# Kernel optimization log

Hardware: AMD Instinct MI355X
Metric: run time of the kernel (lower is better)

## Reference

```python
import jax, jax.numpy as jnp
import numpy as np

N, D, NH, NC, B, NL = 400, 256, 4, 2, 64, 2
HD = D // NH


def _ln(x, g, b, eps=1e-5):
    mu = x.mean(-1, keepdims=True)
    var = ((x - mu) ** 2).mean(-1, keepdims=True)
    return (x - mu) * jax.lax.rsqrt(var + eps) * g + b


def _mha(q, kv, wqkv, bqkv, wo, bo):
    # torch nn.MultiheadAttention (batch_first), eval mode
    wq, wk, wv = jnp.split(wqkv, 3, axis=0)
    bq, bk, bv = jnp.split(bqkv, 3, axis=0)
    Bsz, Sq, _ = q.shape
    Sk = kv.shape[1]
    qh = (q @ wq.T + bq).reshape(Bsz, Sq, NH, HD).transpose(0, 2, 1, 3)
    kh = (kv @ wk.T + bk).reshape(Bsz, Sk, NH, HD).transpose(0, 2, 1, 3)
    vh = (kv @ wv.T + bv).reshape(Bsz, Sk, NH, HD).transpose(0, 2, 1, 3)
    scores = jnp.einsum('bhqd,bhkd->bhqk', qh, kh) / jnp.sqrt(jnp.float32(HD))
    attn = jax.nn.softmax(scores, axis=-1)
    o = jnp.einsum('bhqk,bhkd->bhqd', attn, vh)
    o = o.transpose(0, 2, 1, 3).reshape(Bsz, Sq, D)
    return o @ wo.T + bo


def setup_inputs() -> dict:
    key = jax.random.key(0)
    ks = iter(jax.random.split(key, 64))
    w = lambda *s: (jax.random.normal(next(ks), s, dtype=jnp.float32) * 0.02)
    inp = {
        'fc_matrix': jax.random.uniform(next(ks), (B, N, N), dtype=jnp.float32),
        'sc_matrix': jax.random.uniform(next(ks), (B, N, N), dtype=jnp.float32),
        'proj_w': w(D, N), 'proj_b': jnp.zeros((D,), jnp.float32),
        'enc_qkv_w': w(NL, 3 * D, D), 'enc_qkv_b': jnp.zeros((NL, 3 * D), jnp.float32),
        'enc_out_w': w(NL, D, D), 'enc_out_b': jnp.zeros((NL, D), jnp.float32),
        'enc_lin1_w': w(NL, 4 * D, D), 'enc_lin1_b': jnp.zeros((NL, 4 * D), jnp.float32),
        'enc_lin2_w': w(NL, D, 4 * D), 'enc_lin2_b': jnp.zeros((NL, D), jnp.float32),
        'enc_n1_g': jnp.ones((NL, D), jnp.float32), 'enc_n1_b': jnp.zeros((NL, D), jnp.float32),
        'enc_n2_g': jnp.ones((NL, D), jnp.float32), 'enc_n2_b': jnp.zeros((NL, D), jnp.float32),
        'gcn_w1': w(D, N), 'gcn_b1': jnp.zeros((D,), jnp.float32),
        'gcn_w2': w(D, D), 'gcn_b2': jnp.zeros((D,), jnp.float32),
        'ca1_qkv_w': w(3 * D, D), 'ca1_qkv_b': jnp.zeros((3 * D,), jnp.float32),
        'ca1_out_w': w(D, D), 'ca1_out_b': jnp.zeros((D,), jnp.float32),
        'ca1_n_g': jnp.ones((D,), jnp.float32), 'ca1_n_b': jnp.zeros((D,), jnp.float32),
        'ca2_qkv_w': w(3 * D, D), 'ca2_qkv_b': jnp.zeros((3 * D,), jnp.float32),
        'ca2_out_w': w(D, D), 'ca2_out_b': jnp.zeros((D,), jnp.float32),
        'ca2_n_g': jnp.ones((D,), jnp.float32), 'ca2_n_b': jnp.zeros((D,), jnp.float32),
        'cls_w1': w(128, N * D), 'cls_b1': jnp.zeros((128,), jnp.float32),
        'cls_w2': w(NC, 128), 'cls_b2': jnp.zeros((NC,), jnp.float32),
    }
    return inp


def reference(fc_matrix, sc_matrix, proj_w, proj_b,
              enc_qkv_w, enc_qkv_b, enc_out_w, enc_out_b,
              enc_lin1_w, enc_lin1_b, enc_lin2_w, enc_lin2_b,
              enc_n1_g, enc_n1_b, enc_n2_g, enc_n2_b,
              gcn_w1, gcn_b1, gcn_w2, gcn_b2,
              ca1_qkv_w, ca1_qkv_b, ca1_out_w, ca1_out_b, ca1_n_g, ca1_n_b,
              ca2_qkv_w, ca2_qkv_b, ca2_out_w, ca2_out_b, ca2_n_g, ca2_n_b,
              cls_w1, cls_b1, cls_w2, cls_b2):
    # ---- FC branch: input proj + 2 post-norm transformer encoder layers ----
    h = fc_matrix @ proj_w.T + proj_b  # [B,N,D]
    for l in range(NL):
        a = _mha(h, h, enc_qkv_w[l], enc_qkv_b[l], enc_out_w[l], enc_out_b[l])
        h = _ln(h + a, enc_n1_g[l], enc_n1_b[l])
        ff = jax.nn.relu(h @ enc_lin1_w[l].T + enc_lin1_b[l]) @ enc_lin2_w[l].T + enc_lin2_b[l]
        h = _ln(h + ff, enc_n2_g[l], enc_n2_b[l])
    Z_F = h

    # ---- SC branch: dense-equivalent of per-sample nonzero()+GCNConv ----
    # all entries of sc are nonzero -> edge set == dense adjacency (self-loops present,
    # so add_remaining_self_loops is a no-op). deg = in-degree (column sums of weights).
    deg = sc_matrix.sum(axis=-2)  # [B,N]
    dinv = jnp.where(deg > 0, jax.lax.rsqrt(deg), 0.0)
    An = dinv[:, :, None] * sc_matrix * dinv[:, None, :]  # An[b,i,j] = dinv_i * w_ij * dinv_j
    h1 = jnp.einsum('bij,bid->bjd', An, sc_matrix @ gcn_w1.T) + gcn_b1  # aggregate src->dst
    h1 = jax.nn.relu(h1)
    Z_S = jnp.einsum('bij,bid->bjd', An, h1 @ gcn_w2.T) + gcn_b2  # [B,N,D]

    # ---- Cross attention (eval: dropout = identity) ----
    Z_F_cross = _ln(Z_F + _mha(Z_F, Z_S, ca1_qkv_w, ca1_qkv_b, ca1_out_w, ca1_out_b), ca1_n_g, ca1_n_b)
    Z_S_cross = _ln(Z_S + _mha(Z_S, Z_F, ca2_qkv_w, ca2_qkv_b, ca2_out_w, ca2_out_b), ca2_n_g, ca2_n_b)

    Z_joint = (Z_F_cross + Z_S_cross) * 0.5
    flat = Z_joint.reshape(Z_joint.shape[0], -1)  # [B, N*D]
    logits = jax.nn.relu(flat @ cls_w1.T + cls_b1) @ cls_w2.T + cls_b2
    return logits
```

## Files before the change

kernel.cpp:

```cpp
#include <hip/hip_runtime.h>
#include <math.h>

#define NB   64
#define NN   400
#define DD   256
#define NHH  4
#define HDD  64
#define MR   25600

typedef __attribute__((ext_vector_type(8))) short bf16x8;
typedef __attribute__((ext_vector_type(4))) float f32x4;

__device__ __forceinline__ short f2bf(float x) {
    union { float f; unsigned u; } v; v.f = x;
    return (short)((v.u + 0x7FFFu + ((v.u >> 16) & 1u)) >> 16);
}
__device__ __forceinline__ float bf2f(short s) {
    union { unsigned u; float f; } v; v.u = ((unsigned)(unsigned short)s) << 16;
    return v.f;
}
__device__ __forceinline__ void gl_lds16(const void* g, void* l) {
    __builtin_amdgcn_global_load_lds(
        (const __attribute__((address_space(1))) unsigned*)g,
        (__attribute__((address_space(3))) unsigned*)l, 16, 0, 0);
}
__device__ __forceinline__ void wait_vmcnt(int n) {
    switch (n) {
    case 0: asm volatile("s_waitcnt vmcnt(0)" ::: "memory"); break;
    case 1: asm volatile("s_waitcnt vmcnt(1)" ::: "memory"); break;
    case 2: asm volatile("s_waitcnt vmcnt(2)" ::: "memory"); break;
    case 3: asm volatile("s_waitcnt vmcnt(3)" ::: "memory"); break;
    case 4: asm volatile("s_waitcnt vmcnt(4)" ::: "memory"); break;
    default: asm volatile("s_waitcnt vmcnt(5)" ::: "memory"); break;
    }
}
__device__ __forceinline__ void barrier_raw() {
    __builtin_amdgcn_sched_barrier(0);
    __builtin_amdgcn_s_barrier();
    __builtin_amdgcn_sched_barrier(0);
}


__global__ __launch_bounds__(512, 4) void gemm_p8(
    const short* __restrict__ A, int arows, long long sA,
    const short* __restrict__ B, int brows, long long sB,
    const float* __restrict__ bias,
    short* __restrict__ C, int crows, int crz, long long sCe,
    int M, int N, int Npad, int K, int relu)
{
    __shared__ short lds[36864];
    const int tid = threadIdx.x;

    const unsigned gx = gridDim.x, gy = gridDim.y;
    const unsigned nwg = gx * gy * gridDim.z;
    const unsigned lin = (blockIdx.z * gy + blockIdx.y) * gx + blockIdx.x;
    const unsigned g = (lin & 7) * (nwg >> 3) + (lin >> 3);
    const unsigned zz = g / (gx * gy);
    const unsigned rem2 = g - zz * gx * gy;
    const unsigned mx = rem2 / gy;
    const unsigned ny = rem2 - mx * gy;

    const int z = (int)zz;
    const int m0 = (int)mx * 256, n0 = (int)ny * 128;
    const short* Ab = A + (size_t)z * sA;
    const short* Bb = B + (size_t)z * sB;

    const int w = tid >> 6, lane = tid & 63;
    const int quad = lane >> 4, l15 = lane & 15;
    const int wm = w & 3, wn = w >> 2;

    f32x4 acc[4][4] = {};

    const int KT = K >> 5;

    auto STAGE = [&](int buf, int kt) {
        const int gp0 = kt << 2;
        short* Al = lds + buf * 12288;
        short* Bl = Al + 8192;
#pragma unroll
        for (int i = 0; i < 3; ++i) {
            int c = i * 8 + w;
            if (c < 16) {
                int p = c >> 2, hh = c & 3;
                gl_lds16(Ab + ((size_t)(gp0 + p) * arows + m0 + hh * 64 + lane) * 8,
                         &Al[(p * 256 + hh * 64) * 8]);
            } else {
                int cb = c - 16, p = cb >> 1, hh = cb & 1;
                gl_lds16(Bb + ((size_t)(gp0 + p) * brows + n0 + hh * 64 + lane) * 8,
                         &Bl[(p * 128 + hh * 64) * 8]);
            }
        }
    };

    STAGE(0, 0);
    STAGE(1, 1);
    for (int kt = 0; kt < KT; ++kt) {
        wait_vmcnt(kt + 1 < KT ? 3 : 0);
        barrier_raw();
        if (kt + 2 < KT) STAGE((kt + 2) % 3, kt + 2);
        const short* Al = lds + (kt % 3) * 12288;
        const short* Bl = Al + 8192;
        bf16x8 af[4], bfr[4];
#pragma unroll
        for (int mi = 0; mi < 4; ++mi)
            af[mi] = *reinterpret_cast<const bf16x8*>(
                &Al[(quad * 256 + wm * 64 + mi * 16 + l15) * 8]);
#pragma unroll
        for (int ni = 0; ni < 4; ++ni)
            bfr[ni] = *reinterpret_cast<const bf16x8*>(
                &Bl[(quad * 128 + wn * 64 + ni * 16 + l15) * 8]);
#pragma unroll
        for (int mi = 0; mi < 4; ++mi)
#pragma unroll
            for (int ni = 0; ni < 4; ++ni)
                acc[mi][ni] = __builtin_amdgcn_mfma_f32_16x16x32_bf16(af[mi], bfr[ni], acc[mi][ni], 0, 0, 0);
    }
    __syncthreads();

#pragma unroll
    for (int mi = 0; mi < 4; ++mi) {
#pragma unroll
        for (int r = 0; r < 4; ++r) {
            int row = wm * 64 + mi * 16 + quad * 4 + r;
#pragma unroll
            for (int ni = 0; ni < 4; ++ni) {
                int col = wn * 64 + ni * 16 + l15;
                int gcol = n0 + col;
                float v = 0.0f;
                if (gcol < N) {
                    v = acc[mi][ni][r];
                    if (bias) v += bias[gcol];
                    if (relu) v = fmaxf(v, 0.0f);
                }
                lds[row * 136 + col] = f2bf(v);
            }
        }
    }
    __syncthreads();
    short* Cbz = C + (size_t)z * sCe;
    const long long zr = (long long)z * crz;
#pragma unroll
    for (int t = 0; t < 8; ++t) {
        int c = t * 512 + tid;
        int row = c & 255, p16 = c >> 8;
        int grow = m0 + row;
        int gcol0 = n0 + p16 * 8;
        if (grow < M && gcol0 < Npad) {
            bf16x8 v = *reinterpret_cast<const bf16x8*>(&lds[row * 136 + p16 * 8]);
            *reinterpret_cast<bf16x8*>(
                &Cbz[((size_t)(gcol0 >> 3) * crows + zr + grow) * 8]) = v;
        }
    }
}

__global__ __launch_bounds__(512, 4) void gemm_ln(
    const short* __restrict__ A,
    const short* __restrict__ B, int brows,
    const float* __restrict__ bias,
    const short* __restrict__ resid,
    const float* __restrict__ g, const float* __restrict__ bb,
    short* __restrict__ out, int K)
{
    __shared__ short lds[30720];
    __shared__ float gs[256], bs[256], bi_s[256];
    __shared__ float red[2][8][64];
    const int tid = threadIdx.x;
    const int m0 = blockIdx.x * 64;
    const int w = tid >> 6, lane = tid & 63;
    const int quad = lane >> 4, l15 = lane & 15;
    if (tid < 256) { gs[tid] = g[tid]; bs[tid] = bb[tid]; bi_s[tid] = bias[tid]; }

    f32x4 acc[4][2] = {};
    const int KT = K >> 5;
    const int myloads = (w < 4) ? 3 : 2;

    auto STAGE = [&](int buf, int kt) {
        const int gp0 = kt << 2;
        short* Al = lds + buf * 10240;
        short* Bl = Al + 2048;
#pragma unroll
        for (int i = 0; i < 3; ++i) {
            int c = i * 8 + w;
            if (c < 4) {
                gl_lds16(A + ((size_t)(gp0 + c) * MR + m0 + lane) * 8, &Al[(c * 64) * 8]);
            } else if (c < 20) {
                int cb = c - 4, p = cb >> 2, cq = cb & 3;
                gl_lds16(B + ((size_t)(gp0 + p) * brows + cq * 64 + lane) * 8,
                         &Bl[(p * 256 + cq * 64) * 8]);
            }
        }
    };

    STAGE(0, 0);
    STAGE(1, 1);
    for (int kt = 0; kt < KT; ++kt) {
        wait_vmcnt(kt + 1 < KT ? myloads : 0);
        barrier_raw();
        if (kt + 2 < KT) STAGE((kt + 2) % 3, kt + 2);
        const short* Al = lds + (kt % 3) * 10240;
        const short* Bl = Al + 2048;
        bf16x8 af[4], bfr[2];
#pragma unroll
        for (int mi = 0; mi < 4; ++mi)
            af[mi] = *reinterpret_cast<const bf16x8*>(
                &Al[(quad * 64 + mi * 16 + l15) * 8]);
#pragma unroll
        for (int ni = 0; ni < 2; ++ni)
            bfr[ni] = *reinterpret_cast<const bf16x8*>(
                &Bl[(quad * 256 + w * 32 + ni * 16 + l15) * 8]);
#pragma unroll
        for (int mi = 0; mi < 4; ++mi)
#pragma unroll
            for (int ni = 0; ni < 2; ++ni)
                acc[mi][ni] = __builtin_amdgcn_mfma_f32_16x16x32_bf16(af[mi], bfr[ni], acc[mi][ni], 0, 0, 0);
    }
    __syncthreads();

    short* rowt = lds;
#pragma unroll
    for (int mi = 0; mi < 4; ++mi)
#pragma unroll
        for (int ni = 0; ni < 2; ++ni) {
            int col = w * 32 + ni * 16 + l15;
            int part = col >> 6, idx = col & 63;
#pragma unroll
            for (int r = 0; r < 4; ++r) {
                int row = mi * 16 + quad * 4 + r;
                rowt[row * 264 + part * 66 + idx] = f2bf(acc[mi][ni][r] + bi_s[col]);
            }
        }
    __syncthreads();

    const int row = tid >> 3, part = tid & 7;
    const int grow = m0 + row;
    float vv[4][8];
    float sum = 0.0f, sq = 0.0f;
#pragma unroll
    for (int i = 0; i < 4; ++i) {
        int plane = part * 4 + i;
        bf16x8 rv = *reinterpret_cast<const bf16x8*>(resid + ((size_t)plane * MR + grow) * 8);
        bf16x8 tv = *reinterpret_cast<const bf16x8*>(
            &rowt[row * 264 + (plane >> 3) * 66 + (plane & 7) * 8]);
#pragma unroll
        for (int e = 0; e < 8; ++e) {
            float v = bf2f(tv[e]) + bf2f(rv[e]);
            vv[i][e] = v; sum += v; sq += v * v;
        }
    }
    red[0][part][row] = sum; red[1][part][row] = sq;
    __syncthreads();
    sum = 0.0f; sq = 0.0f;
#pragma unroll
    for (int p = 0; p < 8; ++p) { sum += red[0][p][row]; sq += red[1][p][row]; }
    float mu = sum * (1.0f / 256.0f);
    float var = sq * (1.0f / 256.0f) - mu * mu;
    float rstd = 1.0f / sqrtf(fmaxf(var, 0.0f) + 1e-5f);
#pragma unroll
    for (int i = 0; i < 4; ++i) {
        int plane = part * 4 + i;
        bf16x8 o;
#pragma unroll
        for (int e = 0; e < 8; ++e)
            o[e] = f2bf((vv[i][e] - mu) * rstd * gs[plane * 8 + e] + bs[plane * 8 + e]);
        *reinterpret_cast<bf16x8*>(out + ((size_t)plane * MR + grow) * 8) = o;
    }
}

__global__ __launch_bounds__(256) void vtrans(
    const short* __restrict__ qkv, short* __restrict__ vT)
{
    __shared__ short tile[64][66];
    const int id = blockIdx.x;
    const int xcd = id & 7, rem = id >> 3;
    const int bh_hi = rem / 7, c = rem - bh_hi * 7;
    const int bh_i = bh_hi * 8 + xcd;
    const int h = bh_i & 3, b = bh_i >> 2;
    const int tid = threadIdx.x;
    const size_t bh = (size_t)bh_i;
    for (int t = tid; t < 512; t += 256) {
        int pp = t >> 6, l = t & 63;
        int j = c * 64 + l;
        bf16x8 v;
        if (j < NN)
            v = *reinterpret_cast<const bf16x8*>(
                qkv + (((size_t)(64 + 8 * h + pp)) * MR + (size_t)b * NN + j) * 8);
        else { for (int e = 0; e < 8; ++e) v[e] = 0; }
#pragma unroll
        for (int e = 0; e < 8; ++e) tile[l][pp * 8 + e] = v[e];
    }
    __syncthreads();
    for (int t = tid; t < 512; t += 256) {
        int kq = t >> 6, d = t & 63;
        int kp = c * 8 + kq;
        bf16x8 o;
#pragma unroll
        for (int e = 0; e < 8; ++e) o[e] = tile[kq * 8 + e][d];
        *reinterpret_cast<bf16x8*>(vT + ((bh * 56 + kp) * 64 + d) * 8) = o;
    }
}

__global__ __launch_bounds__(256, 3) void attn_p8(
    const short* __restrict__ qkv, const short* __restrict__ vT,
    short* __restrict__ Out)
{
    __shared__ short PS[26624];
    const int id = blockIdx.x;
    const int xcd = id & 7, rem = id >> 3;
    const int bh_hi = rem / 7, qt = rem - bh_hi * 7;
    const int bh_i = bh_hi * 8 + xcd;
    const int h = bh_i & 3, b = bh_i >> 2;
    const int tid = threadIdx.x;
    const int w = tid >> 6, lane = tid & 63;
    const int quad = lane >> 4, l15 = lane & 15;
    const size_t rowb = (size_t)b * NN;

    for (int j = w; j < 8; j += 4)
        gl_lds16(qkv + (((size_t)(8 * h + j)) * MR + rowb + qt * 64 + lane) * 8, &PS[j * 512]);
    __syncthreads();

    bf16x8 aq0 = *reinterpret_cast<const bf16x8*>(&PS[(quad * 64 + w * 16 + l15) * 8]);
    bf16x8 aq1 = *reinterpret_cast<const bf16x8*>(&PS[((4 + quad) * 64 + w * 16 + l15) * 8]);

    const short* Kb0 = qkv + ((size_t)(32 + 8 * h + quad) * MR + rowb + l15) * 8;
    const short* Kb1 = qkv + ((size_t)(36 + 8 * h + quad) * MR + rowb + l15) * 8;

    f32x4 sacc[25];
#pragma unroll
    for (int nt = 0; nt < 25; ++nt) { sacc[nt][0] = 0; sacc[nt][1] = 0; sacc[nt][2] = 0; sacc[nt][3] = 0; }
#pragma unroll
    for (int nt = 0; nt < 25; ++nt) {
        bf16x8 b0 = *reinterpret_cast<const bf16x8*>(Kb0 + nt * 128);
        bf16x8 b1 = *reinterpret_cast<const bf16x8*>(Kb1 + nt * 128);
        sacc[nt] = __builtin_amdgcn_mfma_f32_16x16x32_bf16(aq0, b0, sacc[nt], 0, 0, 0);
        sacc[nt] = __builtin_amdgcn_mfma_f32_16x16x32_bf16(aq1, b1, sacc[nt], 0, 0, 0);
    }

    float mx[4] = {-3e38f, -3e38f, -3e38f, -3e38f}, sm[4] = {0, 0, 0, 0};
#pragma unroll
    for (int nt = 0; nt < 25; ++nt)
#pragma unroll
        for (int r = 0; r < 4; ++r) mx[r] = fmaxf(mx[r], sacc[nt][r]);
#pragma unroll
    for (int r = 0; r < 4; ++r) {
        mx[r] = fmaxf(mx[r], __shfl_xor(mx[r], 1));
        mx[r] = fmaxf(mx[r], __shfl_xor(mx[r], 2));
        mx[r] = fmaxf(mx[r], __shfl_xor(mx[r], 4));
        mx[r] = fmaxf(mx[r], __shfl_xor(mx[r], 8));
    }
#pragma unroll
    for (int nt = 0; nt < 25; ++nt)
#pragma unroll
        for (int r = 0; r < 4; ++r) {
            float e = __expf((sacc[nt][r] - mx[r]) * 0.125f);
            sacc[nt][r] = e;
            sm[r] += e;
        }
#pragma unroll
    for (int r = 0; r < 4; ++r) {
        sm[r] += __shfl_xor(sm[r], 1);
        sm[r] += __shfl_xor(sm[r], 2);
        sm[r] += __shfl_xor(sm[r], 4);
        sm[r] += __shfl_xor(sm[r], 8);
    }
    __syncthreads();

#pragma unroll
    for (int nt = 0; nt < 25; ++nt)
#pragma unroll
        for (int r = 0; r < 4; ++r) {
            int colk = nt * 16 + l15;
            PS[((colk >> 3) * 64 + w * 16 + quad * 4 + r) * 8 + (colk & 7)] = f2bf(sacc[nt][r]);
        }
    for (int idx = tid; idx < 1024; idx += 256) PS[25600 + idx] = 0;

    f32x4 oacc[4];
#pragma unroll
    for (int dt = 0; dt < 4; ++dt) { oacc[dt][0] = 0; oacc[dt][1] = 0; oacc[dt][2] = 0; oacc[dt][3] = 0; }
    __syncthreads();

    const short* Vb = vT + (((size_t)bh_i * 56 + quad) * 64 + l15) * 8;
#pragma unroll
    for (int kt = 0; kt < 13; ++kt) {
        bf16x8 pa = *reinterpret_cast<const bf16x8*>(
            &PS[((kt * 4 + quad) * 64 + w * 16 + l15) * 8]);
#pragma unroll
        for (int dt = 0; dt < 4; ++dt) {
            bf16x8 vb = *reinterpret_cast<const bf16x8*>(Vb + kt * 2048 + dt * 128);
            oacc[dt] = __builtin_amdgcn_mfma_f32_16x16x32_bf16(pa, vb, oacc[dt], 0, 0, 0);
        }
    }
#pragma unroll
    for (int r = 0; r < 4; ++r) {
        int row = qt * 64 + w * 16 + quad * 4 + r;
        if (row >= NN) continue;
        float inv = 1.0f / sm[r];
#pragma unroll
        for (int dt = 0; dt < 4; ++dt) {
            int col = dt * 16 + l15;
            Out[(((size_t)(8 * h + (col >> 3))) * MR + rowb + row) * 8 + (col & 7)] =
                f2bf(oacc[dt][r] * inv);
        }
    }
}

__global__ void conv_p8(const float* __restrict__ src, short* __restrict__ dst,
                        int R, int K, int Kp, int PR)
{
    const int G = Kp >> 3;
    int idx = blockIdx.x * 256 + threadIdx.x;
    if (idx >= R * G) return;
    int r = idx / G, g = idx - r * G;
    int k0 = g << 3;
    bf16x8 o;
    if (k0 + 8 <= K) {
        const float4 v0 = *reinterpret_cast<const float4*>(src + (size_t)r * K + k0);
        const float4 v1 = *reinterpret_cast<const float4*>(src + (size_t)r * K + k0 + 4);
        o[0] = f2bf(v0.x); o[1] = f2bf(v0.y); o[2] = f2bf(v0.z); o[3] = f2bf(v0.w);
        o[4] = f2bf(v1.x); o[5] = f2bf(v1.y); o[6] = f2bf(v1.z); o[7] = f2bf(v1.w);
    } else {
#pragma unroll
        for (int e = 0; e < 8; ++e) {
            int k = k0 + e;
            o[e] = (k < K) ? f2bf(src[(size_t)r * K + k]) : (short)0;
        }
    }
    *reinterpret_cast<bf16x8*>(dst + ((size_t)g * PR + r) * 8) = o;
}

struct ConvSeg { const float* src; short* dst; int R, K, Kp, start; };
struct ConvPack { ConvSeg s[11]; int total; };

__global__ void conv_multi(ConvPack p)
{
    int idx = blockIdx.x * 256 + threadIdx.x;
    if (idx >= p.total) return;
    int si = 0;
#pragma unroll
    for (int t = 1; t < 11; ++t) if (idx >= p.s[t].start) si = t;
    const ConvSeg sg = p.s[si];
    int local = idx - sg.start;
    const int G = sg.Kp >> 3;
    int r = local / G, g = local - r * G;
    int k0 = g << 3;
    bf16x8 o;
    if (k0 + 8 <= sg.K) {
        const float4 v0 = *reinterpret_cast<const float4*>(sg.src + (size_t)r * sg.K + k0);
        const float4 v1 = *reinterpret_cast<const float4*>(sg.src + (size_t)r * sg.K + k0 + 4);
        o[0] = f2bf(v0.x); o[1] = f2bf(v0.y); o[2] = f2bf(v0.z); o[3] = f2bf(v0.w);
        o[4] = f2bf(v1.x); o[5] = f2bf(v1.y); o[6] = f2bf(v1.z); o[7] = f2bf(v1.w);
    } else {
#pragma unroll
        for (int e = 0; e < 8; ++e) {
            int k = k0 + e;
            o[e] = (k < sg.K) ? f2bf(sg.src[(size_t)r * sg.K + k]) : (short)0;
        }
    }
    *reinterpret_cast<bf16x8*>(sg.dst + ((size_t)g * sg.R + r) * 8) = o;
}

__global__ __launch_bounds__(256) void w1_p8(
    const float* __restrict__ W1, short* __restrict__ Wp)
{
    __shared__ float tile[128][129];
    const int k0 = blockIdx.x * 128;
    const int tid = threadIdx.x;
    for (int t = 0; t < 16; ++t) {
        int idx = t * 256 + tid;
        int r = idx >> 5, k4 = idx & 31;
        float4 v = *(const float4*)(W1 + (size_t)r * 102400 + k0 + k4 * 4);
        tile[r][k4 * 4 + 0] = v.x; tile[r][k4 * 4 + 1] = v.y;
        tile[r][k4 * 4 + 2] = v.z; tile[r][k4 * 4 + 3] = v.w;
    }
    __syncthreads();
    for (int t = 0; t < 8; ++t) {
        int idx = t * 256 + tid;
        int pidx = idx >> 7, r = idx & 127;
        bf16x8 o;
#pragma unroll
        for (int e = 0; e < 8; ++e) o[e] = f2bf(tile[r][pidx * 8 + e]);
        *reinterpret_cast<bf16x8*>(Wp + (((size_t)(k0 >> 3) + pidx) * 128 + r) * 8) = o;
    }
}

__global__ void colsum_dinv(const float* __restrict__ sc, float* __restrict__ dinv)
{
    int b = blockIdx.y;
    int j = blockIdx.x * 256 + threadIdx.x;
    if (j >= NN) return;
    const float* p = sc + (size_t)b * NN * NN + j;
    float s = 0.0f;
    for (int i = 0; i < NN; ++i) s += p[(size_t)i * NN];
    dinv[b * NN + j] = (s > 0.0f) ? 1.0f / sqrtf(s) : 0.0f;
}

__global__ __launch_bounds__(256) void sc_prep(
    const float* __restrict__ sc, const float* __restrict__ dinv,
    short* __restrict__ scb, short* __restrict__ anT)
{
    __shared__ float tile[64][65];
    const int b = blockIdx.z;
    const int i0 = blockIdx.y * 64, j0 = blockIdx.x * 64;
    const int tid = threadIdx.x;
    const float* sb = sc + (size_t)b * NN * NN;
    short* scbb = scb + (size_t)b * 56 * 512 * 8;
    short* anTb = anT + (size_t)b * 56 * 512 * 8;
    for (int e = tid; e < 4096; e += 256) {
        int r = e >> 6, c = e & 63;
        int i = i0 + r, j = j0 + c;
        tile[r][c] = (i < NN && j < NN) ? sb[(size_t)i * NN + j] : 0.0f;
    }
    __syncthreads();
    for (int e = tid; e < 4096; e += 256) {
        int r = e >> 6, c = e & 63;
        int i = i0 + r, j = j0 + c;
        scbb[((size_t)(j >> 3) * 512 + i) * 8 + (j & 7)] = f2bf(tile[r][c]);
        float v = 0.0f;
        if (i < NN && j < NN) v = tile[r][c] * dinv[b * NN + i] * dinv[b * NN + j];
        anTb[((size_t)(i >> 3) * 512 + j) * 8 + (i & 7)] = f2bf(v);
    }
}

__global__ __launch_bounds__(256) void cls_gemm(
    const short* __restrict__ C1, const short* __restrict__ C2,
    const short* __restrict__ Wp, float* __restrict__ partial)
{
    __shared__ short Al[32 * 64 * 8];
    __shared__ short Wl[8 * 128 * 8];
    const int j = blockIdx.x;
    const int tid = threadIdx.x;
    const int w = tid >> 6, lane = tid & 63;
    const int quad = lane >> 4, l15 = lane & 15;

    for (int s = 0; s < 8; ++s) {
        int idx = s * 256 + tid;
        int p = idx >> 6, b = idx & 63;
        size_t ad = ((size_t)p * MR + (size_t)b * NN + j) * 8;
        bf16x8 a = *reinterpret_cast<const bf16x8*>(C1 + ad);
        bf16x8 c = *reinterpret_cast<const bf16x8*>(C2 + ad);
        bf16x8 o;
#pragma unroll
        for (int e = 0; e < 8; ++e) o[e] = f2bf(0.5f * (bf2f(a[e]) + bf2f(c[e])));
        *reinterpret_cast<bf16x8*>(&Al[(p * 64 + b) * 8]) = o;
    }

    f32x4 acc[4][2] = {};
    const size_t wp0 = (size_t)j * 32;
    for (int s = 0; s < 4; ++s) {
#pragma unroll
        for (int pp = 0; pp < 2; ++pp) {
            int p = w + pp * 4;
            gl_lds16(Wp + ((wp0 + s * 8 + p) * 128 + lane) * 8,      &Wl[(p * 128) * 8]);
            gl_lds16(Wp + ((wp0 + s * 8 + p) * 128 + 64 + lane) * 8, &Wl[(p * 128 + 64) * 8]);
        }
        __syncthreads();
#pragma unroll
        for (int kb = 0; kb < 2; ++kb) {
            bf16x8 af[4], bfr[2];
#pragma unroll
            for (int mi = 0; mi < 4; ++mi)
                af[mi] = *reinterpret_cast<const bf16x8*>(
                    &Al[((s * 8 + kb * 4 + quad) * 64 + mi * 16 + l15) * 8]);
#pragma unroll
            for (int ni = 0; ni < 2; ++ni)
                bfr[ni] = *reinterpret_cast<const bf16x8*>(
                    &Wl[((kb * 4 + quad) * 128 + w * 32 + ni * 16 + l15) * 8]);
#pragma unroll
            for (int mi = 0; mi < 4; ++mi)
#pragma unroll
                for (int ni = 0; ni < 2; ++ni)
                    acc[mi][ni] = __builtin_amdgcn_mfma_f32_16x16x32_bf16(af[mi], bfr[ni], acc[mi][ni], 0, 0, 0);
        }
        __syncthreads();
    }
    float* pj = partial + (size_t)j * 8192;
#pragma unroll
    for (int mi = 0; mi < 4; ++mi)
#pragma unroll
        for (int r = 0; r < 4; ++r) {
            int row = mi * 16 + quad * 4 + r;
#pragma unroll
            for (int ni = 0; ni < 2; ++ni)
                pj[row * 128 + w * 32 + ni * 16 + l15] = acc[mi][ni][r];
        }
}

__global__ void cls_reduce(const float* __restrict__ partial, float* __restrict__ clsh)
{
    int o = blockIdx.x * 256 + threadIdx.x;
    float s = 0.0f;
    for (int kb = 0; kb < 400; ++kb) s += partial[(size_t)kb * 8192 + o];
    clsh[o] = s;
}

__global__ void logits_final(
    const float* __restrict__ clsh, const float* __restrict__ b1,
    const float* __restrict__ w2, const float* __restrict__ b2,
    float* __restrict__ out)
{
    __shared__ float t[128];
    int b = blockIdx.x;
    int tid = threadIdx.x;
    t[tid] = fmaxf(clsh[b * 128 + tid] + b1[tid], 0.0f);
    __syncthreads();
    if (tid < 2) {
        float s = b2[tid];
        for (int o = 0; o < 128; ++o) s += t[o] * w2[tid * 128 + o];
        out[b * 2 + tid] = s;
    }
}

extern "C" void kernel_launch(void* const* d_in, const int* in_sizes, int n_in,
                              void* d_out, int out_size, void* d_ws, size_t ws_size,
                              hipStream_t stream)
{
    const float* fc        = (const float*)d_in[0];
    const float* sc        = (const float*)d_in[1];
    const float* proj_w    = (const float*)d_in[2];
    const float* proj_b    = (const float*)d_in[3];
    const float* enc_qkv_w = (const float*)d_in[4];
    const float* enc_qkv_b = (const float*)d_in[5];
    const float* enc_out_w = (const float*)d_in[6];
    const float* enc_out_b = (const float*)d_in[7];
    const float* enc_l1_w  = (const float*)d_in[8];
    const float* enc_l1_b  = (const float*)d_in[9];
    const float* enc_l2_w  = (const float*)d_in[10];
    const float* enc_l2_b  = (const float*)d_in[11];
    const float* enc_n1_g  = (const float*)d_in[12];
    const float* enc_n1_b  = (const float*)d_in[13];
    const float* enc_n2_g  = (const float*)d_in[14];
    const float* enc_n2_b  = (const float*)d_in[15];
    const float* gcn_w1    = (const float*)d_in[16];
    const float* gcn_b1    = (const float*)d_in[17];
    const float* gcn_w2    = (const float*)d_in[18];
    const float* gcn_b2    = (const float*)d_in[19];
    const float* ca1_qkv_w = (const float*)d_in[20];
    const float* ca1_qkv_b = (const float*)d_in[21];
    const float* ca1_out_w = (const float*)d_in[22];
    const float* ca1_out_b = (const float*)d_in[23];
    const float* ca1_n_g   = (const float*)d_in[24];
    const float* ca1_n_b   = (const float*)d_in[25];
    const float* ca2_qkv_w = (const float*)d_in[26];
    const float* ca2_qkv_b = (const float*)d_in[27];
    const float* ca2_out_w = (const float*)d_in[28];
    const float* ca2_out_b = (const float*)d_in[29];
    const float* ca2_n_g   = (const float*)d_in[30];
    const float* ca2_n_b   = (const float*)d_in[31];
    const float* cls_w1    = (const float*)d_in[32];
    const float* cls_b1    = (const float*)d_in[33];
    const float* cls_w2    = (const float*)d_in[34];
    const float* cls_b2    = (const float*)d_in[35];

    char* wsb = (char*)d_ws;
    size_t off = 0;
    auto alloc = [&](size_t bytes) { char* r = wsb + off; off += (bytes + 255) & ~(size_t)255; return r; };
    short* bufBig = (short*)alloc((size_t)MR * 1024 * 2);
    short* fcb    = (short*)alloc((size_t)56 * MR * 8 * 2);
    short* anT    = (short*)alloc((size_t)NB * 56 * 512 * 8 * 2);
    short* bufH   = (short*)alloc((size_t)32 * MR * 8 * 2);
    short* bufA   = (short*)alloc((size_t)32 * MR * 8 * 2);
    short* bufC   = (short*)alloc((size_t)32 * MR * 8 * 2);
    short* bufZS  = (short*)alloc((size_t)32 * MR * 8 * 2);
    short* vT     = (short*)alloc((size_t)NB * NHH * 56 * 64 * 8 * 2);
    short* w1b    = (short*)alloc((size_t)12800 * 128 * 8 * 2);
    short* projwb = (short*)alloc((size_t)56 * 256 * 8 * 2);
    short* qkvwb  = (short*)alloc((size_t)32 * 1536 * 8 * 2);
    short* outwb  = (short*)alloc((size_t)32 * 512 * 8 * 2);
    short* l1wb   = (short*)alloc((size_t)32 * 2048 * 8 * 2);
    short* l2wb   = (short*)alloc((size_t)128 * 512 * 8 * 2);
    short* gw1b   = (short*)alloc((size_t)56 * 256 * 8 * 2);
    short* gw2b   = (short*)alloc((size_t)32 * 256 * 8 * 2);
    short* c1qb   = (short*)alloc((size_t)32 * 768 * 8 * 2);
    short* c1ob   = (short*)alloc((size_t)32 * 256 * 8 * 2);
    short* c2qb   = (short*)alloc((size_t)32 * 768 * 8 * 2);
    short* c2ob   = (short*)alloc((size_t)32 * 256 * 8 * 2);
    float* dinv   = (float*)alloc((size_t)MR * 4);
    float* clsh   = (float*)alloc((size_t)NB * 128 * 4);
    short* scb = bufBig;
    short* XT1 = bufBig + (size_t)64 * 56 * 512 * 8;
    short* h1  = bufBig;
    short* XT2 = XT1;
    float* partial = (float*)fcb;

    dim3 blk(256), blk512(512);
    auto cgrid = [](long long n) { return dim3((unsigned)((n + 255) / 256)); };

    conv_p8<<<cgrid((long long)MR * 56), blk, 0, stream>>>(fc, fcb, MR, 400, 448, MR);
    {
        ConvPack pk;
        int st = 0;
        auto seg = [&](int i, const float* s, short* d, int R, int K, int Kp) {
            pk.s[i].src = s; pk.s[i].dst = d; pk.s[i].R = R; pk.s[i].K = K;
            pk.s[i].Kp = Kp; pk.s[i].start = st; st += R * (Kp >> 3);
        };
        seg(0,  proj_w,    projwb, 256,  400,  448);
        seg(1,  enc_qkv_w, qkvwb,  1536, 256,  256);
        seg(2,  enc_out_w, outwb,  512,  256,  256);
        seg(3,  enc_l1_w,  l1wb,   2048, 256,  256);
        seg(4,  enc_l2_w,  l2wb,   512,  1024, 1024);
        seg(5,  gcn_w1,    gw1b,   256,  400,  448);
        seg(6,  gcn_w2,    gw2b,   256,  256,  256);
        seg(7,  ca1_qkv_w, c1qb,   768,  256,  256);
        seg(8,  ca1_out_w, c1ob,   256,  256,  256);
        seg(9,  ca2_qkv_w, c2qb,   768,  256,  256);
        seg(10, ca2_out_w, c2ob,   256,  256,  256);
        pk.total = st;
        conv_multi<<<cgrid(st), blk, 0, stream>>>(pk);
    }
    w1_p8<<<800, blk, 0, stream>>>(cls_w1, w1b);

    gemm_p8<<<dim3(100, 2, 1), blk512, 0, stream>>>(
        fcb, MR, 0, projwb, 256, 0, proj_b, bufH, MR, 0, 0, MR, 256, 256, 448, 0);
    for (int l = 0; l < 2; ++l) {
        gemm_p8<<<dim3(100, 6, 1), blk512, 0, stream>>>(
            bufH, MR, 0, qkvwb + (size_t)l * 768 * 8, 1536, 0, enc_qkv_b + l * 768,
            bufBig, MR, 0, 0, MR, 768, 768, 256, 0);
        vtrans<<<dim3(1792), blk, 0, stream>>>(bufBig, vT);
        attn_p8<<<dim3(1792), blk, 0, stream>>>(bufBig, vT, bufA);
        gemm_ln<<<400, blk512, 0, stream>>>(
            bufA, outwb + (size_t)l * 256 * 8, 512, enc_out_b + l * 256,
            bufH, enc_n1_g + l * DD, enc_n1_b + l * DD, bufH, 256);
        gemm_p8<<<dim3(100, 8, 1), blk512, 0, stream>>>(
            bufH, MR, 0, l1wb + (size_t)l * 1024 * 8, 2048, 0, enc_l1_b + l * 1024,
            bufBig, MR, 0, 0, MR, 1024, 1024, 256, 1);
        gemm_ln<<<400, blk512, 0, stream>>>(
            bufBig, l2wb + (size_t)l * 256 * 8, 512, enc_l2_b + l * 256,
            bufH, enc_n2_g + l * DD, enc_n2_b + l * DD, bufH, 1024);
    }

    colsum_dinv<<<dim3(2, NB), blk, 0, stream>>>(sc, dinv);
    sc_prep<<<dim3(7, 7, NB), blk, 0, stream>>>(sc, dinv, scb, anT);
    gemm_p8<<<dim3(1, 4, NB), blk512, 0, stream>>>(
        gw1b, 256, 0, scb, 512, 56LL * 512 * 8, nullptr,
        XT1, 256, 0, 56LL * 256 * 8, 256, 400, 448, 448, 0);
    gemm_p8<<<dim3(2, 2, NB), blk512, 0, stream>>>(
        anT, 512, 56LL * 512 * 8, XT1, 256, 56LL * 256 * 8, gcn_b1,
        h1, 512, 0, 32LL * 512 * 8, 400, 256, 256, 448, 1);
    gemm_p8<<<dim3(1, 4, NB), blk512, 0, stream>>>(
        gw2b, 256, 0, h1, 512, 32LL * 512 * 8, nullptr,
        XT2, 256, 0, 56LL * 256 * 8, 256, 400, 448, 256, 0);
    gemm_p8<<<dim3(2, 2, NB), blk512, 0, stream>>>(
        anT, 512, 56LL * 512 * 8, XT2, 256, 56LL * 256 * 8, gcn_b2,
        bufZS, MR, 400, 0, 400, 256, 256, 448, 0);

    gemm_p8<<<dim3(100, 2, 1), blk512, 0, stream>>>(
        bufH, MR, 0, c1qb, 768, 0, ca1_qkv_b, bufBig, MR, 0, 0, MR, 256, 256, 256, 0);
    gemm_p8<<<dim3(100, 4, 1), blk512, 0, stream>>>(
        bufZS, MR, 0, c1qb + 256 * 8, 768, 0, ca1_qkv_b + 256,
        bufBig + (size_t)32 * MR * 8, MR, 0, 0, MR, 512, 512, 256, 0);
    vtrans<<<dim3(1792), blk, 0, stream>>>(bufBig, vT);
    attn_p8<<<dim3(1792), blk, 0, stream>>>(bufBig, vT, bufA);
    gemm_ln<<<400, blk512, 0, stream>>>(
        bufA, c1ob, 256, ca1_out_b, bufH, ca1_n_g, ca1_n_b, bufC, 256);

    gemm_p8<<<dim3(100, 2, 1), blk512, 0, stream>>>(
        bufZS, MR, 0, c2qb, 768, 0, ca2_qkv_b, bufBig, MR, 0, 0, MR, 256, 256, 256, 0);
    gemm_p8<<<dim3(100, 4, 1), blk512, 0, stream>>>(
        bufH, MR, 0, c2qb + 256 * 8, 768, 0, ca2_qkv_b + 256,
        bufBig + (size_t)32 * MR * 8, MR, 0, 0, MR, 512, 512, 256, 0);
    vtrans<<<dim3(1792), blk, 0, stream>>>(bufBig, vT);
    attn_p8<<<dim3(1792), blk, 0, stream>>>(bufBig, vT, bufA);
    gemm_ln<<<400, blk512, 0, stream>>>(
        bufA, c2ob, 256, ca2_out_b, bufZS, ca2_n_g, ca2_n_b, bufZS, 256);

    cls_gemm<<<400, blk, 0, stream>>>(bufC, bufZS, w1b, partial);
    cls_reduce<<<32, blk, 0, stream>>>(partial, clsh);
    logits_final<<<NB, 128, 0, stream>>>(clsh, cls_b1, cls_w2, cls_b2, (float*)d_out);
}
```

Baseline: 894.1 us.

## Split attention into single-wave blocks of 16 query rows

```diff
diff --git a/kernel.cpp b/kernel.cpp
--- a/kernel.cpp
+++ b/kernel.cpp
@@ -299,27 +299,25 @@
     }
 }
 
-__global__ __launch_bounds__(256, 3) void attn_p8(
+__global__ __launch_bounds__(64) void attn_p8(
     const short* __restrict__ qkv, const short* __restrict__ vT,
     short* __restrict__ Out)
 {
-    __shared__ short PS[26624];
+    __shared__ short PS[6656];
     const int id = blockIdx.x;
     const int xcd = id & 7, rem = id >> 3;
-    const int bh_hi = rem / 7, qt = rem - bh_hi * 7;
+    const int bh_hi = rem / 25, qt = rem - bh_hi * 25;
     const int bh_i = bh_hi * 8 + xcd;
     const int h = bh_i & 3, b = bh_i >> 2;
-    const int tid = threadIdx.x;
-    const int w = tid >> 6, lane = tid & 63;
+    const int lane = threadIdx.x & 63;
     const int quad = lane >> 4, l15 = lane & 15;
     const size_t rowb = (size_t)b * NN;
-
-    for (int j = w; j < 8; j += 4)
-        gl_lds16(qkv + (((size_t)(8 * h + j)) * MR + rowb + qt * 64 + lane) * 8, &PS[j * 512]);
-    __syncthreads();
-
-    bf16x8 aq0 = *reinterpret_cast<const bf16x8*>(&PS[(quad * 64 + w * 16 + l15) * 8]);
-    bf16x8 aq1 = *reinterpret_cast<const bf16x8*>(&PS[((4 + quad) * 64 + w * 16 + l15) * 8]);
+    const int q0 = qt * 16;
+
+    bf16x8 aq0 = *reinterpret_cast<const bf16x8*>(
+        qkv + (((size_t)(8 * h + quad)) * MR + rowb + q0 + l15) * 8);
+    bf16x8 aq1 = *reinterpret_cast<const bf16x8*>(
+        qkv + (((size_t)(8 * h + 4 + quad)) * MR + rowb + q0 + l15) * 8);
 
     const short* Kb0 = qkv + ((size_t)(32 + 8 * h + quad) * MR + rowb + l15) * 8;
     const short* Kb1 = qkv + ((size_t)(36 + 8 * h + quad) * MR + rowb + l15) * 8;
@@ -362,27 +360,25 @@
         sm[r] += __shfl_xor(sm[r], 4);
         sm[r] += __shfl_xor(sm[r], 8);
     }
-    __syncthreads();
 
 #pragma unroll
     for (int nt = 0; nt < 25; ++nt)
 #pragma unroll
         for (int r = 0; r < 4; ++r) {
             int colk = nt * 16 + l15;
-            PS[((colk >> 3) * 64 + w * 16 + quad * 4 + r) * 8 + (colk & 7)] = f2bf(sacc[nt][r]);
-        }
-    for (int idx = tid; idx < 1024; idx += 256) PS[25600 + idx] = 0;
+            PS[((colk >> 3) * 16 + quad * 4 + r) * 8 + (colk & 7)] = f2bf(sacc[nt][r]);
+        }
+    for (int idx = lane; idx < 256; idx += 64) PS[6400 + idx] = 0;
 
     f32x4 oacc[4];
 #pragma unroll
     for (int dt = 0; dt < 4; ++dt) { oacc[dt][0] = 0; oacc[dt][1] = 0; oacc[dt][2] = 0; oacc[dt][3] = 0; }
-    __syncthreads();
 
     const short* Vb = vT + (((size_t)bh_i * 56 + quad) * 64 + l15) * 8;
 #pragma unroll
     for (int kt = 0; kt < 13; ++kt) {
         bf16x8 pa = *reinterpret_cast<const bf16x8*>(
-            &PS[((kt * 4 + quad) * 64 + w * 16 + l15) * 8]);
+            &PS[((kt * 4 + quad) * 16 + l15) * 8]);
 #pragma unroll
         for (int dt = 0; dt < 4; ++dt) {
             bf16x8 vb = *reinterpret_cast<const bf16x8*>(Vb + kt * 2048 + dt * 128);
@@ -391,8 +387,7 @@
     }
 #pragma unroll
     for (int r = 0; r < 4; ++r) {
-        int row = qt * 64 + w * 16 + quad * 4 + r;
-        if (row >= NN) continue;
+        int row = q0 + quad * 4 + r;
         float inv = 1.0f / sm[r];
 #pragma unroll
         for (int dt = 0; dt < 4; ++dt) {
@@ -681,7 +676,7 @@
     short* XT2 = XT1;
     float* partial = (float*)fcb;
 
-    dim3 blk(256), blk512(512);
+    dim3 blk(256), blk512(512), blk64(64);
     auto cgrid = [](long long n) { return dim3((unsigned)((n + 255) / 256)); };
 
     conv_p8<<<cgrid((long long)MR * 56), blk, 0, stream>>>(fc, fcb, MR, 400, 448, MR);
@@ -715,7 +710,7 @@
             bufH, MR, 0, qkvwb + (size_t)l * 768 * 8, 1536, 0, enc_qkv_b + l * 768,
             bufBig, MR, 0, 0, MR, 768, 768, 256, 0);
         vtrans<<<dim3(1792), blk, 0, stream>>>(bufBig, vT);
-        attn_p8<<<dim3(1792), blk, 0, stream>>>(bufBig, vT, bufA);
+        attn_p8<<<dim3(6400), blk64, 0, stream>>>(bufBig, vT, bufA);
         gemm_ln<<<400, blk512, 0, stream>>>(
             bufA, outwb + (size_t)l * 256 * 8, 512, enc_out_b + l * 256,
             bufH, enc_n1_g + l * DD, enc_n1_b + l * DD, bufH, 256);
@@ -748,7 +743,7 @@
         bufZS, MR, 0, c1qb + 256 * 8, 768, 0, ca1_qkv_b + 256,
         bufBig + (size_t)32 * MR * 8, MR, 0, 0, MR, 512, 512, 256, 0);
     vtrans<<<dim3(1792), blk, 0, stream>>>(bufBig, vT);
-    attn_p8<<<dim3(1792), blk, 0, stream>>>(bufBig, vT, bufA);
+    attn_p8<<<dim3(6400), blk64, 0, stream>>>(bufBig, vT, bufA);
     gemm_ln<<<400, blk512, 0, stream>>>(
         bufA, c1ob, 256, ca1_out_b, bufH, ca1_n_g, ca1_n_b, bufC, 256);
 
@@ -758,7 +753,7 @@
         bufH, MR, 0, c2qb + 256 * 8, 768, 0, ca2_qkv_b + 256,
         bufBig + (size_t)32 * MR * 8, MR, 0, 0, MR, 512, 512, 256, 0);
     vtrans<<<dim3(1792), blk, 0, stream>>>(bufBig, vT);
-    attn_p8<<<dim3(1792), blk, 0, stream>>>(bufBig, vT, bufA);
+    attn_p8<<<dim3(6400), blk64, 0, stream>>>(bufBig, vT, bufA);
     gemm_ln<<<400, blk512, 0, stream>>>(
         bufA, c2ob, 256, ca2_out_b, bufZS, ca2_n_g, ca2_n_b, bufZS, 256);
 
```

Result: no change. 878.1 us (-1.8%).
